# Kernel tuning notes

Measured on AMD Instinct MI355X. Metric: run time of the kernel, lower is better.

Reference implementation:

```python
import jax, jax.numpy as jnp
import numpy as np

H = 20  # hidden size (hardcoded in the torch module)

def setup_inputs() -> dict:
    key = jax.random.key(0)
    ks = jax.random.split(key, 7)
    s = 0.1  # keep activations in a sane range for tanh/sigmoid
    return {
        "x":     jax.random.normal(ks[0], (8192, 512, 12), dtype=jnp.float32),
        "w_ih":  jax.random.normal(ks[1], (4 * H, 12), dtype=jnp.float32) * s,
        "w_hh":  jax.random.normal(ks[2], (4 * H, H), dtype=jnp.float32) * s,
        "b_ih":  jax.random.normal(ks[3], (4 * H,), dtype=jnp.float32) * s,
        "b_hh":  jax.random.normal(ks[4], (4 * H,), dtype=jnp.float32) * s,
        "w_out": jax.random.normal(ks[5], (10, H), dtype=jnp.float32) * s,
        "b_out": jax.random.normal(ks[6], (10,), dtype=jnp.float32) * s,
    }

def reference(x, w_ih, w_hh, b_ih, b_hh, w_out, b_out):
    # x: [B, T, I]. Single-layer LSTM (PyTorch gate order i,f,g,o), zero init state,
    # then Linear on the last hidden state.
    B, T, _ = x.shape
    # Precompute input projections for all timesteps: [T, B, 4H]
    x_proj = jnp.einsum('bti,gi->tbg', x, w_ih) + (b_ih + b_hh)

    def step(carry, xt):
        h, c = carry                      # each [B, H]
        gates = xt + h @ w_hh.T           # [B, 4H]
        i, f, g, o = jnp.split(gates, 4, axis=-1)
        i = jax.nn.sigmoid(i)
        f = jax.nn.sigmoid(f)
        g = jnp.tanh(g)
        o = jax.nn.sigmoid(o)
        c = f * c + i * g
        h = o * jnp.tanh(c)
        return (h, c), None

    h0 = jnp.zeros((B, H), dtype=x.dtype)
    c0 = jnp.zeros((B, H), dtype=x.dtype)
    (h_last, _), _ = jax.lax.scan(step, (h0, c0), x_proj)
    # out = Linear(h_T): r_out[:, -1, :] == h_n for a single-layer LSTM
    return h_last @ w_out.T + b_out
```

## Files before the change

### kernel.cpp

```cpp
#include <hip/hip_runtime.h>

typedef _Float16 f16;
typedef f16   f16x2  __attribute__((ext_vector_type(2)));
typedef f16   f16x8  __attribute__((ext_vector_type(8)));
typedef float f32x4  __attribute__((ext_vector_type(4)));
typedef float f32x4u __attribute__((ext_vector_type(4), aligned(4)));
typedef __fp16 h16x2 __attribute__((ext_vector_type(2)));

#define T_STEPS 512
#define INPUT   12
#define HID     20
#define BATCH   16
#define LOG2E      1.4426950408889634f
#define TWO_LOG2E  2.8853900817779268f

static __device__ __forceinline__ f16x2 pk(float a, float b) {
    h16x2 r = __builtin_amdgcn_cvt_pkrtz(a, b);
    return __builtin_bit_cast(f16x2, r);
}
static __device__ __forceinline__ float sig_pre(float a) {
    return __builtin_amdgcn_rcpf(1.0f + __builtin_amdgcn_exp2f(a));
}
static __device__ __forceinline__ float tanh_pre(float a) {
    return 1.0f - 2.0f * __builtin_amdgcn_rcpf(1.0f + __builtin_amdgcn_exp2f(a));
}

__global__ __launch_bounds__(64) void lstm_kernel(
    const float* __restrict__ x,
    const float* __restrict__ w_ih,
    const float* __restrict__ w_hh,
    const float* __restrict__ b_ih,
    const float* __restrict__ b_hh,
    const float* __restrict__ w_out,
    const float* __restrict__ b_out,
    float* __restrict__ out)
{
    const int lane = threadIdx.x & 63;
    const int col  = lane & 15;
    const int quad = lane >> 4;

    const int   g_row = col & 3;
    const float sA    = (g_row == 2) ? TWO_LOG2E : -LOG2E;

    f16x8 afragW[5];
#pragma unroll
    for (int t = 0; t < 5; ++t) {
        int u_r = 5 * (col >> 2) + t;
        int row = g_row * HID + u_r;
        f16x8 w;
#pragma unroll
        for (int j = 0; j < 8; ++j) {
            float v = (j < 3) ? w_ih[row * INPUT + 3 * quad + j]
                              : w_hh[row * HID + 5 * quad + (j - 3)];
            w[j] = (f16)(v * sA);
        }
        afragW[t] = w;
    }

    f32x4 cbias[5];
#pragma unroll
    for (int t = 0; t < 5; ++t) {
        int u_b = 5 * quad + t;
#pragma unroll
        for (int r = 0; r < 4; ++r) {
            float s = (r == 2) ? TWO_LOG2E : -LOG2E;
            cbias[t][r] = (b_ih[r * HID + u_b] + b_hh[r * HID + u_b]) * s;
        }
    }

    const int al_words = (quad == 0) ? 0 : (quad == 1) ? 2 : (quad == 2) ? 6 : 8;
    const int sel      = quad & 1;
    const float* xp = x + (size_t)(blockIdx.x * BATCH + col) * (T_STEPS * INPUT) + al_words;

    auto loadx = [&](int t) -> f32x4 {
        return *(const f32x4u*)(xp + (size_t)t * INPUT);
    };

    union BF { f16x8 v; f16x2 h2[4]; } bf;
    {
        f32x4 xv = loadx(0);
        float x0 = sel ? xv[1] : xv[0];
        float x1 = sel ? xv[2] : xv[1];
        float x2 = sel ? xv[3] : xv[2];
        bf.h2[0] = pk(x0, x1);
        bf.h2[1] = pk(x2, 0.f);
        bf.h2[2] = pk(0.f, 0.f);
        bf.h2[3] = pk(0.f, 0.f);
    }

    float cst[5] = {0.f, 0.f, 0.f, 0.f, 0.f};

    f32x4 qA = loadx(1);
    f32x4 qB = loadx(2);

    auto step = [&](f32x4& q, int tl) {
        f32x4 acc[5];
#pragma unroll
        for (int t = 0; t < 5; ++t)
            acc[t] = __builtin_amdgcn_mfma_f32_16x16x32_f16(afragW[t], bf.v, cbias[t], 0, 0, 0);

        float h[5];
#pragma unroll
        for (int t = 0; t < 5; ++t) {
            float ig = sig_pre(acc[t][0]);
            float fg = sig_pre(acc[t][1]);
            float gg = tanh_pre(acc[t][2]);
            float og = sig_pre(acc[t][3]);
            float c2 = fg * cst[t] + ig * gg;
            cst[t] = c2;
            h[t] = og * tanh_pre(TWO_LOG2E * c2);
        }

        float x0 = sel ? q[1] : q[0];
        float x1 = sel ? q[2] : q[1];
        float x2 = sel ? q[3] : q[2];
        q = loadx(tl);

        bf.h2[0] = pk(x0, x1);
        bf.h2[1] = pk(x2, h[0]);
        bf.h2[2] = pk(h[1], h[2]);
        bf.h2[3] = pk(h[3], h[4]);
    };

#pragma unroll 1
    for (int t = 0; t < T_STEPS; t += 2) {
        int l1 = t + 3; if (l1 > T_STEPS - 1) l1 = T_STEPS - 1;
        int l2 = t + 4; if (l2 > T_STEPS - 1) l2 = T_STEPS - 1;
        step(qA, l1);
        step(qB, l2);
    }

    __shared__ f16 htmp[BATCH][HID];
    htmp[col][5 * quad + 0] = bf.h2[1][1];
    htmp[col][5 * quad + 1] = bf.h2[2][0];
    htmp[col][5 * quad + 2] = bf.h2[2][1];
    htmp[col][5 * quad + 3] = bf.h2[3][0];
    htmp[col][5 * quad + 4] = bf.h2[3][1];
    __syncthreads();

#pragma unroll
    for (int base = 0; base < BATCH * 10; base += 64) {
        int idx = base + lane;
        if (idx < BATCH * 10) {
            int b = idx / 10, o = idx % 10;
            float s = b_out[o];
#pragma unroll
            for (int u = 0; u < HID; ++u)
                s += (float)htmp[b][u] * w_out[o * HID + u];
            out[(size_t)(blockIdx.x * BATCH + b) * 10 + o] = s;
        }
    }
}

extern "C" void kernel_launch(void* const* d_in, const int* in_sizes, int n_in,
                              void* d_out, int out_size, void* d_ws, size_t ws_size,
                              hipStream_t stream) {
    const float* x     = (const float*)d_in[0];
    const float* w_ih  = (const float*)d_in[1];
    const float* w_hh  = (const float*)d_in[2];
    const float* b_ih  = (const float*)d_in[3];
    const float* b_hh  = (const float*)d_in[4];
    const float* w_out = (const float*)d_in[5];
    const float* b_out = (const float*)d_in[6];
    float* out = (float*)d_out;

    const int blocks = 8192 / BATCH;
    hipLaunchKernelGGL(lstm_kernel, dim3(blocks), dim3(64), 0, stream,
                       x, w_ih, w_hh, b_ih, b_hh, w_out, b_out, out);
}
```

Measured before the change: 444.3 us.

## Split LSTM hidden units across two wavefronts with LDS-exchanged hidden state

Splits the 5 MFMA tiles per step across two wavefronts per block (3 tiles each, one padded) instead of one wavefront doing all 5. The hidden state now travels through a double-buffered LDS array with a block barrier every timestep, rather than staying in registers. Gate nonlinearities are restructured to share reciprocals, computing two sigmoids from one rcp. This shortens the serial per-step chain per wave, at the cost of LDS traffic, a barrier per step, and a wasted padded tile.

```diff
diff --git a/kernel.cpp b/kernel.cpp
--- a/kernel.cpp
+++ b/kernel.cpp
@@ -11,21 +11,20 @@
 #define INPUT   12
 #define HID     20
 #define BATCH   16
+#define HSTR    25
 #define LOG2E      1.4426950408889634f
 #define TWO_LOG2E  2.8853900817779268f
 
+static __device__ __forceinline__ void block_barrier() {
+    asm volatile("s_waitcnt lgkmcnt(0)\n\ts_barrier" ::: "memory");
+}
+static __device__ __forceinline__ f16 cvt16(float a) { return (f16)a; }
 static __device__ __forceinline__ f16x2 pk(float a, float b) {
     h16x2 r = __builtin_amdgcn_cvt_pkrtz(a, b);
     return __builtin_bit_cast(f16x2, r);
 }
-static __device__ __forceinline__ float sig_pre(float a) {
-    return __builtin_amdgcn_rcpf(1.0f + __builtin_amdgcn_exp2f(a));
-}
-static __device__ __forceinline__ float tanh_pre(float a) {
-    return 1.0f - 2.0f * __builtin_amdgcn_rcpf(1.0f + __builtin_amdgcn_exp2f(a));
-}
 
-__global__ __launch_bounds__(64) void lstm_kernel(
+__global__ __launch_bounds__(128) void lstm_kernel(
     const float* __restrict__ x,
     const float* __restrict__ w_ih,
     const float* __restrict__ w_hh,
@@ -35,118 +34,121 @@
     const float* __restrict__ b_out,
     float* __restrict__ out)
 {
-    const int lane = threadIdx.x & 63;
+    __shared__ f16 H[2][BATCH][HSTR];
+
+    const int tid  = threadIdx.x;
+    const int wid  = tid >> 6;
+    const int lane = tid & 63;
     const int col  = lane & 15;
     const int quad = lane >> 4;
+
+    {
+        f16* h0 = &H[0][0][0];
+        for (int i = tid; i < BATCH * HSTR; i += 128) h0[i] = (f16)0.f;
+    }
 
     const int   g_row = col & 3;
     const float sA    = (g_row == 2) ? TWO_LOG2E : -LOG2E;
 
-    f16x8 afragW[5];
+    f16x8 afragW[3];
+    f32x4 cbias[3];
+    int   uu[3];
 #pragma unroll
-    for (int t = 0; t < 5; ++t) {
-        int u_r = 5 * (col >> 2) + t;
-        int row = g_row * HID + u_r;
-        f16x8 w;
+    for (int tt = 0; tt < 3; ++tt) {
+        const int T = 3 * wid + tt;
+        uu[tt] = 4 * T + quad;
+        f16x8 w = {};
+        f32x4 cb = {};
+        if (T < 5) {
+            const int u_r = 4 * T + (col >> 2);
+            const int row = g_row * HID + u_r;
 #pragma unroll
-        for (int j = 0; j < 8; ++j) {
-            float v = (j < 3) ? w_ih[row * INPUT + 3 * quad + j]
-                              : w_hh[row * HID + 5 * quad + (j - 3)];
-            w[j] = (f16)(v * sA);
+            for (int j = 0; j < 8; ++j) {
+                float v = (j < 3) ? w_ih[row * INPUT + 3 * quad + j]
+                                  : w_hh[row * HID + 5 * quad + (j - 3)];
+                w[j] = (f16)(v * sA);
+            }
+            const int u_b = 4 * T + quad;
+#pragma unroll
+            for (int r = 0; r < 4; ++r) {
+                float s = (r == 2) ? TWO_LOG2E : -LOG2E;
+                cb[r] = (b_ih[r * HID + u_b] + b_hh[r * HID + u_b]) * s;
+            }
         }
-        afragW[t] = w;
-    }
-
-    f32x4 cbias[5];
-#pragma unroll
-    for (int t = 0; t < 5; ++t) {
-        int u_b = 5 * quad + t;
-#pragma unroll
-        for (int r = 0; r < 4; ++r) {
-            float s = (r == 2) ? TWO_LOG2E : -LOG2E;
-            cbias[t][r] = (b_ih[r * HID + u_b] + b_hh[r * HID + u_b]) * s;
-        }
+        afragW[tt] = w;
+        cbias[tt]  = cb;
     }
 
     const int al_words = (quad == 0) ? 0 : (quad == 1) ? 2 : (quad == 2) ? 6 : 8;
     const int sel      = quad & 1;
     const float* xp = x + (size_t)(blockIdx.x * BATCH + col) * (T_STEPS * INPUT) + al_words;
+    auto loadx = [&](int t) -> f32x4 { return *(const f32x4u*)(xp + (size_t)t * INPUT); };
 
-    auto loadx = [&](int t) -> f32x4 {
-        return *(const f32x4u*)(xp + (size_t)t * INPUT);
-    };
+    f32x4 q0 = loadx(0);
+    f32x4 q1 = loadx(1);
 
-    union BF { f16x8 v; f16x2 h2[4]; } bf;
-    {
-        f32x4 xv = loadx(0);
-        float x0 = sel ? xv[1] : xv[0];
-        float x1 = sel ? xv[2] : xv[1];
-        float x2 = sel ? xv[3] : xv[2];
-        bf.h2[0] = pk(x0, x1);
-        bf.h2[1] = pk(x2, 0.f);
-        bf.h2[2] = pk(0.f, 0.f);
-        bf.h2[3] = pk(0.f, 0.f);
-    }
+    float cst[3] = {0.f, 0.f, 0.f};
 
-    float cst[5] = {0.f, 0.f, 0.f, 0.f, 0.f};
+    block_barrier();
 
-    f32x4 qA = loadx(1);
-    f32x4 qB = loadx(2);
+    union BF { f16x8 v; f16 e[8]; f16x2 h2[4]; } bf;
 
-    auto step = [&](f32x4& q, int tl) {
-        f32x4 acc[5];
-#pragma unroll
-        for (int t = 0; t < 5; ++t)
-            acc[t] = __builtin_amdgcn_mfma_f32_16x16x32_f16(afragW[t], bf.v, cbias[t], 0, 0, 0);
-
-        float h[5];
-#pragma unroll
-        for (int t = 0; t < 5; ++t) {
-            float ig = sig_pre(acc[t][0]);
-            float fg = sig_pre(acc[t][1]);
-            float gg = tanh_pre(acc[t][2]);
-            float og = sig_pre(acc[t][3]);
-            float c2 = fg * cst[t] + ig * gg;
-            cst[t] = c2;
-            h[t] = og * tanh_pre(TWO_LOG2E * c2);
-        }
+    auto step = [&](int p, f32x4& q, int tl) {
+        const f16* hr = &H[p][col][5 * quad];
+        f16 hv0 = hr[0], hv1 = hr[1], hv2 = hr[2], hv3 = hr[3], hv4 = hr[4];
 
         float x0 = sel ? q[1] : q[0];
         float x1 = sel ? q[2] : q[1];
         float x2 = sel ? q[3] : q[2];
+        bf.h2[0] = pk(x0, x1);
+        bf.e[2] = cvt16(x2);
+        bf.e[3] = hv0; bf.e[4] = hv1; bf.e[5] = hv2; bf.e[6] = hv3; bf.e[7] = hv4;
+
         q = loadx(tl);
 
-        bf.h2[0] = pk(x0, x1);
-        bf.h2[1] = pk(x2, h[0]);
-        bf.h2[2] = pk(h[1], h[2]);
-        bf.h2[3] = pk(h[3], h[4]);
+        f16* hw = &H[p ^ 1][col][0];
+#pragma unroll
+        for (int tt = 0; tt < 3; ++tt) {
+            f32x4 acc = __builtin_amdgcn_mfma_f32_16x16x32_f16(afragW[tt], bf.v, cbias[tt], 0, 0, 0);
+            float ei = __builtin_amdgcn_exp2f(acc[0]);
+            float ef = __builtin_amdgcn_exp2f(acc[1]);
+            float eg = __builtin_amdgcn_exp2f(acc[2]);
+            float eo = __builtin_amdgcn_exp2f(acc[3]);
+            float di = 1.0f + ei, df = 1.0f + ef;
+            float dg = 1.0f + eg, dn = 1.0f + eo;
+            float r1 = __builtin_amdgcn_rcpf(di * df);
+            float r2 = __builtin_amdgcn_rcpf(dg * dn);
+            float ig = r1 * df;
+            float fg = r1 * di;
+            float og = r2 * dg;
+            float tg = __builtin_fmaf(-2.0f, r2 * dn, 1.0f);
+            float c2 = __builtin_fmaf(fg, cst[tt], ig * tg);
+            cst[tt] = c2;
+            float ec = __builtin_amdgcn_exp2f(TWO_LOG2E * c2);
+            float rc = __builtin_amdgcn_rcpf(1.0f + ec);
+            float h  = og * __builtin_fmaf(-2.0f, rc, 1.0f);
+            hw[uu[tt]] = cvt16(h);
+        }
+        block_barrier();
     };
 
 #pragma unroll 1
     for (int t = 0; t < T_STEPS; t += 2) {
+        int l0 = t + 2; if (l0 > T_STEPS - 1) l0 = T_STEPS - 1;
         int l1 = t + 3; if (l1 > T_STEPS - 1) l1 = T_STEPS - 1;
-        int l2 = t + 4; if (l2 > T_STEPS - 1) l2 = T_STEPS - 1;
-        step(qA, l1);
-        step(qB, l2);
+        step(0, q0, l0);
+        step(1, q1, l1);
     }
 
-    __shared__ f16 htmp[BATCH][HID];
-    htmp[col][5 * quad + 0] = bf.h2[1][1];
-    htmp[col][5 * quad + 1] = bf.h2[2][0];
-    htmp[col][5 * quad + 2] = bf.h2[2][1];
-    htmp[col][5 * quad + 3] = bf.h2[3][0];
-    htmp[col][5 * quad + 4] = bf.h2[3][1];
-    __syncthreads();
-
 #pragma unroll
-    for (int base = 0; base < BATCH * 10; base += 64) {
-        int idx = base + lane;
+    for (int base = 0; base < BATCH * 10; base += 128) {
+        int idx = base + tid;
         if (idx < BATCH * 10) {
             int b = idx / 10, o = idx % 10;
             float s = b_out[o];
 #pragma unroll
             for (int u = 0; u < HID; ++u)
-                s += (float)htmp[b][u] * w_out[o * HID + u];
+                s += (float)H[0][b][u] * w_out[o * HID + u];
             out[(size_t)(blockIdx.x * BATCH + b) * 10 + o] = s;
         }
     }
@@ -165,6 +167,6 @@
     float* out = (float*)d_out;
 
     const int blocks = 8192 / BATCH;
-    hipLaunchKernelGGL(lstm_kernel, dim3(blocks), dim3(64), 0, stream,
+    hipLaunchKernelGGL(lstm_kernel, dim3(blocks), dim3(128), 0, stream,
                        x, w_ih, w_hh, b_ih, b_hh, w_out, b_out, out);
 }
```

New measurement: 495.5 us. 11.5% more time.
